# Kernel optimization log

Hardware: AMD Instinct MI355X
Metric: run time of the kernel (lower is better)

Reference implementation:

```python
import jax, jax.numpy as jnp
import numpy as np

N_NODES = 50000
N_EDGES = 1600000
IN_C = 256
HID_C = 128
OUT_C = 16
HEADS = 8
NEG_SLOPE = 0.2  # PyG GATConv default


def gat_layer(x, src, dst, W, att_src, att_dst, bias, heads, out_c):
    """PyG-style GATConv (eval mode, add_self_loops already applied to src/dst).
    x: [N, F_in], W: [F_in, heads*out_c], att_*: [heads, out_c], bias: [heads*out_c].
    Returns concatenated heads: [N, heads*out_c]."""
    N = x.shape[0]
    h = (x @ W).reshape(N, heads, out_c)                  # [N, H, C]
    a_src = (h * att_src[None]).sum(-1)                   # [N, H]
    a_dst = (h * att_dst[None]).sum(-1)                   # [N, H]
    alpha = a_src[src] + a_dst[dst]                       # [E, H]
    alpha = jax.nn.leaky_relu(alpha, NEG_SLOPE)
    # segment softmax over incoming edges of each destination node
    amax = jax.ops.segment_max(alpha, dst, num_segments=N)  # [N, H]
    alpha = jnp.exp(alpha - jax.lax.stop_gradient(amax)[dst])
    denom = jax.ops.segment_sum(alpha, dst, num_segments=N)  # [N, H]
    w = alpha / denom[dst]                                # [E, H]
    msg = h[src] * w[:, :, None]                          # [E, H, C]
    out = jax.ops.segment_sum(msg, dst, num_segments=N)   # [N, H, C]
    return out.reshape(N, heads * out_c) + bias


def setup_inputs() -> dict:
    key = jax.random.key(0)
    ks = jax.random.split(key, 10)
    x = jax.random.normal(ks[0], (N_NODES, IN_C), dtype=jnp.float32)
    edge_index = jax.random.randint(ks[1], (2, N_EDGES), 0, N_NODES, dtype=jnp.int32)
    c1 = HID_C // HEADS  # 16 per head
    s1 = 1.0 / np.sqrt(IN_C)
    s2 = 1.0 / np.sqrt(HID_C)
    return {
        "x": x,
        "edge_index": edge_index,
        "W1": jax.random.normal(ks[2], (IN_C, HEADS * c1), dtype=jnp.float32) * s1,
        "att_src1": jax.random.normal(ks[3], (HEADS, c1), dtype=jnp.float32) * s1,
        "att_dst1": jax.random.normal(ks[4], (HEADS, c1), dtype=jnp.float32) * s1,
        "bias1": jnp.zeros((HEADS * c1,), dtype=jnp.float32),
        "W2": jax.random.normal(ks[5], (HID_C, OUT_C), dtype=jnp.float32) * s2,
        "att_src2": jax.random.normal(ks[6], (1, OUT_C), dtype=jnp.float32) * s2,
        "att_dst2": jax.random.normal(ks[7], (1, OUT_C), dtype=jnp.float32) * s2,
        "bias2": jnp.zeros((OUT_C,), dtype=jnp.float32),
    }


def reference(x, edge_index, W1, att_src1, att_dst1, bias1, W2, att_src2, att_dst2, bias2):
    N = x.shape[0]
    loop = jnp.arange(N, dtype=edge_index.dtype)
    src = jnp.concatenate([edge_index[0], loop])  # add_self_loops=True (PyG default)
    dst = jnp.concatenate([edge_index[1], loop])
    h = gat_layer(x, src, dst, W1, att_src1, att_dst1, bias1, HEADS, HID_C // HEADS)
    h = jax.nn.relu(h)
    # F.dropout with training=False is identity (eval mode)
    out = gat_layer(h, src, dst, W2, att_src2, att_dst2, bias2, 1, OUT_C)
    return out
```

## Files before the change

kernel.cpp:

```cpp
#include <hip/hip_runtime.h>
#include <hip/hip_bf16.h>


#define NN 50000
#define NE 1600000
#define NBK 196
#define NB_SC 512
#define CHUNK (NE / NB_SC)
#define GB1 782
#define GB2 1563

typedef __attribute__((ext_vector_type(8))) short bf16x8;
typedef __attribute__((ext_vector_type(4))) float f32x4;

__device__ __forceinline__ float lrelu(float x) { return fmaxf(x, 0.2f * x); }

__device__ __forceinline__ float ldf(const void* p, int i, int isbf) {
  return isbf ? __bfloat162float(((const __hip_bfloat16*)p)[i])
              : ((const float*)p)[i];
}
__device__ __forceinline__ short f2bf_bits(float v) {
  __hip_bfloat16 h = __float2bfloat16(v);
  return *reinterpret_cast<short*>(&h);
}
__device__ __forceinline__ float bfs2f(short b) {
  unsigned int u = ((unsigned int)(unsigned short)b) << 16;
  union { unsigned int u; float f; } c; c.u = u; return c.f;
}
__device__ __forceinline__ unsigned short f2h_bits(float v) {
  _Float16 h = (_Float16)v;
  return *reinterpret_cast<unsigned short*>(&h);
}
__device__ __forceinline__ float h2f(unsigned short b) {
  _Float16 h = *reinterpret_cast<_Float16*>(&b);
  return (float)h;
}

#define OFF_H1   ((size_t)0)
#define OFF_H    ((size_t)25600000)
#define OFF_H2   ((size_t)51200000)
#define OFF_AS1  ((size_t)54400000)
#define OFF_AD1  ((size_t)56000000)
#define OFF_AS2  ((size_t)57600000)
#define OFF_AD2  ((size_t)57800000)
#define OFF_CNT  ((size_t)58000000)
#define OFF_OFFS ((size_t)58400000)
#define OFF_CSR  ((size_t)58600000)
#define OFF_WP1  ((size_t)65000000)
#define OFF_TOT  ((size_t)65065536)
#define OFF_FLAG ((size_t)65068608)

__global__ void repack_w1(const void* __restrict__ W1, short* __restrict__ Wp,
                          const unsigned int* __restrict__ xw, int* __restrict__ flag) {
  __shared__ int s[256];
  __shared__ int sf;
  int t = threadIdx.x;
  unsigned int w = xw[t * 97 + 5];
  unsigned int e = (w >> 7) & 0xFF;
  s[t] = (e >= 116 && e <= 138) ? 1 : 0;
  __syncthreads();
  for (int off = 128; off > 0; off >>= 1) {
    if (t < off) s[t] += s[t + off];
    __syncthreads();
  }
  if (t == 0) {
    sf = (s[0] >= 128) ? 1 : 0;
    if (blockIdx.x == 0) *flag = sf;
  }
  __syncthreads();
  int f = sf;
  int i = blockIdx.x * 256 + t;
  int j = i & 7, q = (i >> 3) & 3, c = (i >> 5) & 127, tt = i >> 12;
  int src = (tt * 32 + q * 8 + j) * 128 + c;
  Wp[i] = f ? ((const short*)W1)[src] : f2bf_bits(((const float*)W1)[src]);
}

__global__ __launch_bounds__(256) void fat1(const void* __restrict__ X,
                                            const short* __restrict__ Wp,
                                            short* __restrict__ H1b,
                                            const int* __restrict__ flag,
                                            const int* __restrict__ dst,
                                            int* __restrict__ HB) {
  __shared__ int h[224];
  if (blockIdx.x < GB1) {
    int wave = threadIdx.x >> 6, lane = threadIdx.x & 63;
    int rowbase = blockIdx.x * 64 + wave * 16;
    int l15 = lane & 15, quad = lane >> 4;
    int f = *flag;
    int arow = rowbase + l15;
    if (arow >= NN) arow = NN - 1;
    f32x4 acc[8];
#pragma unroll
    for (int ct = 0; ct < 8; ++ct) acc[ct] = (f32x4){0.f, 0.f, 0.f, 0.f};
    size_t abase = (size_t)arow * 256 + quad * 8;
#pragma unroll
    for (int kt = 0; kt < 8; ++kt) {
      bf16x8 a;
      if (f) {
        a = *(const bf16x8*)((const short*)X + abase + kt * 32);
      } else {
        const float* xp = (const float*)X + abase + kt * 32;
        float4 v0 = *(const float4*)xp, v1 = *(const float4*)(xp + 4);
        a[0] = f2bf_bits(v0.x); a[1] = f2bf_bits(v0.y);
        a[2] = f2bf_bits(v0.z); a[3] = f2bf_bits(v0.w);
        a[4] = f2bf_bits(v1.x); a[5] = f2bf_bits(v1.y);
        a[6] = f2bf_bits(v1.z); a[7] = f2bf_bits(v1.w);
      }
#pragma unroll
      for (int ct = 0; ct < 8; ++ct) {
        bf16x8 b = *(const bf16x8*)(Wp + ((kt * 128 + ct * 16 + l15) * 4 + quad) * 8);
        acc[ct] = __builtin_amdgcn_mfma_f32_16x16x32_bf16(a, b, acc[ct], 0, 0, 0);
      }
    }
    int r0 = rowbase + quad * 4;
#pragma unroll
    for (int ct = 0; ct < 8; ++ct)
#pragma unroll
      for (int r = 0; r < 4; ++r) {
        int row = r0 + r;
        if (row < NN) H1b[(size_t)row * 128 + ct * 16 + l15] = f2bf_bits(acc[ct][r]);
      }
  } else {
    int b = blockIdx.x - GB1;
    int t = threadIdx.x;
    for (int i = t; i < 224; i += 256) h[i] = 0;
    __syncthreads();
    int e0 = b * CHUNK, e1 = e0 + CHUNK;
    for (int e = e0 + t; e < e1; e += 256) atomicAdd(&h[dst[e] >> 8], 1);
    __syncthreads();
    for (int i = t; i < NBK; i += 256) HB[b * NBK + i] = h[i];
  }
}

__global__ __launch_bounds__(256) void fat2(const short* __restrict__ H1b,
                                            const void* __restrict__ as1,
                                            const void* __restrict__ ad1,
                                            float* __restrict__ AS,
                                            float* __restrict__ AD,
                                            const int* __restrict__ flag,
                                            int* __restrict__ HB,
                                            int* __restrict__ total) {
  __shared__ float s_as[128], s_ad[128];
  __shared__ int ts[256];
  int t = threadIdx.x;
  if (blockIdx.x < GB2) {
    int f = *flag;
    if (t < 128) { s_as[t] = ldf(as1, t, f); s_ad[t] = ldf(ad1, t, f); }
    __syncthreads();
    int tid = blockIdx.x * 256 + t;
    if (tid >= NN * 8) return;
    int n = tid >> 3, hh = tid & 7;
    const bf16x8* hp = (const bf16x8*)(H1b + (size_t)n * 128 + hh * 16);
    bf16x8 v0 = hp[0], v1 = hp[1];
    float as = 0.f, ad = 0.f;
#pragma unroll
    for (int i = 0; i < 8; ++i) {
      int b = hh * 16 + i;
      float x0 = bfs2f(v0[i]), x1 = bfs2f(v1[i]);
      as += x0 * s_as[b] + x1 * s_as[b + 8];
      ad += x0 * s_ad[b] + x1 * s_ad[b + 8];
    }
    AS[tid] = as; AD[tid] = ad;
  } else {
    int k = blockIdx.x - GB2;
    int v0 = HB[(t * 2) * NBK + k], v1 = HB[(t * 2 + 1) * NBK + k];
    int s = v0 + v1;
    ts[t] = s;
    __syncthreads();
    for (int off = 1; off < 256; off <<= 1) {
      int a = (t >= off) ? ts[t - off] : 0;
      __syncthreads();
      ts[t] += a;
      __syncthreads();
    }
    int ex = ts[t] - s;
    HB[(t * 2) * NBK + k] = ex;
    HB[(t * 2 + 1) * NBK + k] = ex + v0;
    if (t == 255) total[k] = ts[255];
  }
}

__global__ __launch_bounds__(256) void scat_write(const int* __restrict__ src,
                                                  const int* __restrict__ dst,
                                                  const int* __restrict__ HB,
                                                  const int* __restrict__ total,
                                                  unsigned int* __restrict__ EPp) {
  __shared__ int h[224], sc[256], lofs[224], lc[224], gd[224];
  __shared__ unsigned int EB[CHUNK];
  __shared__ unsigned char BKT[CHUNK];
  int t = threadIdx.x, b = blockIdx.x;
  int tv = (t < NBK) ? total[t] : 0;
  sc[t] = tv;
  __syncthreads();
  for (int off = 1; off < 256; off <<= 1) {
    int a = (t >= off) ? sc[t - off] : 0;
    __syncthreads();
    sc[t] += a;
    __syncthreads();
  }
  if (t < NBK) gd[t] = (sc[t] - tv) + HB[b * NBK + t];
  for (int i = t; i < 224; i += 256) h[i] = 0;
  __syncthreads();
  int e0 = b * CHUNK, e1 = e0 + CHUNK;
  for (int e = e0 + t; e < e1; e += 256) atomicAdd(&h[dst[e] >> 8], 1);
  __syncthreads();
  int v = (t < NBK) ? h[t] : 0;
  sc[t] = v;
  __syncthreads();
  for (int off = 1; off < 256; off <<= 1) {
    int a = (t >= off) ? sc[t - off] : 0;
    __syncthreads();
    sc[t] += a;
    __syncthreads();
  }
  if (t < NBK) { int ex = sc[t] - v; lofs[t] = ex; lc[t] = ex; }
  __syncthreads();
  for (int e = e0 + t; e < e1; e += 256) {
    int d = dst[e];
    int k = d >> 8;
    int pos = atomicAdd(&lc[k], 1);
    EB[pos] = ((unsigned int)(d & 255) << 16) | (unsigned int)src[e];
    BKT[pos] = (unsigned char)k;
  }
  __syncthreads();
  for (int pos = t; pos < CHUNK; pos += 256) {
    int k = BKT[pos];
    EPp[gd[k] + (pos - lofs[k])] = EB[pos];
  }
}

__global__ __launch_bounds__(1024) void bucket_csr(const unsigned int* __restrict__ EPp,
                                                   const int* __restrict__ total,
                                                   int* __restrict__ cnt,
                                                   int* __restrict__ offs,
                                                   unsigned short* __restrict__ csr) {
  __shared__ int h[256], sc[256], lc[256];
  int b = blockIdx.x, t = threadIdx.x;
  int tv = 0;
  if (t < 256) { tv = (t < NBK) ? total[t] : 0; sc[t] = tv; }
  __syncthreads();
  for (int off = 1; off < 256; off <<= 1) {
    int a = (t >= off && t < 256) ? sc[t - off] : 0;
    __syncthreads();
    if (t < 256) sc[t] += a;
    __syncthreads();
  }
  __shared__ int s_gbase, s_n;
  if (t == (unsigned)b) { s_gbase = sc[b] - tv; s_n = tv; }
  __syncthreads();
  int gbase = s_gbase, n = s_n;
  if (t < 256) h[t] = 0;
  __syncthreads();
  for (int i = t; i < n; i += 1024) atomicAdd(&h[(EPp[gbase + i] >> 16) & 255], 1);
  __syncthreads();
  int v = 0;
  if (t < 256) { v = h[t]; sc[t] = v; }
  __syncthreads();
  for (int off = 1; off < 256; off <<= 1) {
    int add = (t >= off && t < 256) ? sc[t - off] : 0;
    __syncthreads();
    if (t < 256) sc[t] += add;
    __syncthreads();
  }
  if (t < 256) {
    int ex = sc[t] - v;
    int node = (b << 8) + t;
    if (node < NN) { cnt[node] = v; offs[node] = gbase + ex; }
    lc[t] = ex;
  }
  __syncthreads();
  for (int i = t; i < n; i += 1024) {
    unsigned int p = EPp[gbase + i];
    int pos = atomicAdd(&lc[(p >> 16) & 255], 1);
    csr[gbase + pos] = (unsigned short)(p & 0xFFFF);
  }
}

__global__ __launch_bounds__(256) void agg1(const short* __restrict__ H1b,
                                            const float* __restrict__ AS,
                                            const float* __restrict__ AD,
                                            const int* __restrict__ offs,
                                            const int* __restrict__ cnt,
                                            const unsigned short* __restrict__ csr,
                                            const void* __restrict__ bias1,
                                            short* __restrict__ Hb,
                                            const int* __restrict__ flag) {
  int lane = threadIdx.x & 63;
  int node = blockIdx.x * 4 + (threadIdx.x >> 6);
  int f = *flag;
  int start = offs[node], deg = cnt[node];
  int g = lane >> 3, k = lane & 7;
  float adst = AD[node * 8 + k];
  float acc[16];
#pragma unroll
  for (int i = 0; i < 16; ++i) acc[i] = 0.f;
  float dsum = 0.f;
  if (g == 0) {
    float p = __expf(lrelu(AS[node * 8 + k] + adst));
    dsum = p;
    const bf16x8* hp = (const bf16x8*)(H1b + (size_t)node * 128 + k * 16);
    bf16x8 v0 = hp[0], v1 = hp[1];
#pragma unroll
    for (int i = 0; i < 8; ++i) {
      acc[i] = p * bfs2f(v0[i]);
      acc[8 + i] = p * bfs2f(v1[i]);
    }
  }
  int s = (g < deg) ? (int)csr[start + g] : -1;
  float a_c = 0.f; bf16x8 v0, v1;
  if (s >= 0) {
    a_c = AS[s * 8 + k];
    const bf16x8* hp = (const bf16x8*)(H1b + (size_t)s * 128 + k * 16);
    v0 = hp[0]; v1 = hp[1];
  }
  for (int eb = 0; eb < deg; eb += 8) {
    int en = eb + 8 + g;
    int sn = (en < deg) ? (int)csr[start + en] : -1;
    float a_n = 0.f; bf16x8 w0, w1;
    if (sn >= 0) {
      a_n = AS[sn * 8 + k];
      const bf16x8* hp = (const bf16x8*)(H1b + (size_t)sn * 128 + k * 16);
      w0 = hp[0]; w1 = hp[1];
    }
    if (s >= 0) {
      float p = __expf(lrelu(a_c + adst));
      dsum += p;
#pragma unroll
      for (int i = 0; i < 8; ++i) {
        acc[i] += p * bfs2f(v0[i]);
        acc[8 + i] += p * bfs2f(v1[i]);
      }
    }
    s = sn; a_c = a_n; v0 = w0; v1 = w1;
  }
#pragma unroll
  for (int i = 0; i < 16; ++i) {
    acc[i] += __shfl_xor(acc[i], 8);
    acc[i] += __shfl_xor(acc[i], 16);
    acc[i] += __shfl_xor(acc[i], 32);
  }
  dsum += __shfl_xor(dsum, 8);
  dsum += __shfl_xor(dsum, 16);
  dsum += __shfl_xor(dsum, 32);
  if (g == 0) {
    float inv = 1.0f / dsum;
    int c0 = k * 16;
    bf16x8 o0, o1;
#pragma unroll
    for (int i = 0; i < 8; ++i) {
      o0[i] = f2bf_bits(fmaxf(acc[i] * inv + ldf(bias1, c0 + i, f), 0.f));
      o1[i] = f2bf_bits(fmaxf(acc[8 + i] * inv + ldf(bias1, c0 + 8 + i, f), 0.f));
    }
    *(bf16x8*)(Hb + (size_t)node * 128 + c0) = o0;
    *(bf16x8*)(Hb + (size_t)node * 128 + c0 + 8) = o1;
  }
}

__global__ __launch_bounds__(256) void gemm2_a2(const short* __restrict__ Hb,
                                                const void* __restrict__ W2,
                                                const void* __restrict__ as2,
                                                const void* __restrict__ ad2,
                                                unsigned short* __restrict__ H2h,
                                                float* __restrict__ AS2,
                                                float* __restrict__ AD2,
                                                const int* __restrict__ flag) {
  __shared__ float sW[2048];
  __shared__ float s_as[16], s_ad[16];
  int t = threadIdx.x;
  int f = *flag;
  for (int i = t; i < 2048; i += 256) sW[i] = ldf(W2, i, f);
  if (t < 16) { s_as[t] = ldf(as2, t, f); s_ad[t] = ldf(ad2, t, f); }
  __syncthreads();
  int n = blockIdx.x * 16 + (t >> 4), c = t & 15;
  const bf16x8* hp = (const bf16x8*)(Hb + (size_t)n * 128);
  float acc = 0.f;
#pragma unroll 4
  for (int k8 = 0; k8 < 16; ++k8) {
    bf16x8 v = hp[k8];
#pragma unroll
    for (int i = 0; i < 8; ++i) acc += bfs2f(v[i]) * sW[(k8 * 8 + i) * 16 + c];
  }
  H2h[n * 16 + c] = f2h_bits(acc);
  float vs = acc * s_as[c], vd = acc * s_ad[c];
#pragma unroll
  for (int off = 1; off < 16; off <<= 1) {
    vs += __shfl_xor(vs, off);
    vd += __shfl_xor(vd, off);
  }
  if (c == 0) { AS2[n] = vs; AD2[n] = vd; }
}

__global__ __launch_bounds__(256) void agg2(const unsigned short* __restrict__ H2h,
                                            const float* __restrict__ AS2,
                                            const float* __restrict__ AD2,
                                            const int* __restrict__ offs,
                                            const int* __restrict__ cnt,
                                            const unsigned short* __restrict__ csr,
                                            const void* __restrict__ bias2,
                                            void* __restrict__ outv,
                                            const int* __restrict__ flag) {
  int lane = threadIdx.x & 63;
  int node = blockIdx.x * 4 + (threadIdx.x >> 6);
  int f = *flag;
  int start = offs[node], deg = cnt[node];
  int g = lane >> 3, k = lane & 7;
  float adst = AD2[node];
  float a0 = 0.f, a1 = 0.f, dsum = 0.f;
  if (g == 0) {
    float p = __expf(lrelu(AS2[node] + adst));
    dsum = p;
    unsigned int hv = *(const unsigned int*)(H2h + (size_t)node * 16 + k * 2);
    a0 = p * h2f((unsigned short)(hv & 0xFFFF));
    a1 = p * h2f((unsigned short)(hv >> 16));
  }
  int s = (g < deg) ? (int)csr[start + g] : -1;
  float as_c = 0.f; unsigned int hv_c = 0;
  if (s >= 0) {
    as_c = AS2[s];
    hv_c = *(const unsigned int*)(H2h + (size_t)s * 16 + k * 2);
  }
  for (int eb = 0; eb < deg; eb += 8) {
    int en = eb + 8 + g;
    int sn = (en < deg) ? (int)csr[start + en] : -1;
    float as_n = 0.f; unsigned int hv_n = 0;
    if (sn >= 0) {
      as_n = AS2[sn];
      hv_n = *(const unsigned int*)(H2h + (size_t)sn * 16 + k * 2);
    }
    if (s >= 0) {
      float p = __expf(lrelu(as_c + adst));
      dsum += p;
      a0 += p * h2f((unsigned short)(hv_c & 0xFFFF));
      a1 += p * h2f((unsigned short)(hv_c >> 16));
    }
    s = sn; as_c = as_n; hv_c = hv_n;
  }
  a0 += __shfl_xor(a0, 8);  a0 += __shfl_xor(a0, 16);  a0 += __shfl_xor(a0, 32);
  a1 += __shfl_xor(a1, 8);  a1 += __shfl_xor(a1, 16);  a1 += __shfl_xor(a1, 32);
  dsum += __shfl_xor(dsum, 8); dsum += __shfl_xor(dsum, 16); dsum += __shfl_xor(dsum, 32);
  if (g == 0) {
    float inv = 1.0f / dsum;
    float o0 = a0 * inv + ldf(bias2, k * 2 + 0, f);
    float o1 = a1 * inv + ldf(bias2, k * 2 + 1, f);
    size_t base = (size_t)node * 16 + k * 2;
    if (f) {
      ((__hip_bfloat16*)outv)[base] = __float2bfloat16(o0);
      ((__hip_bfloat16*)outv)[base + 1] = __float2bfloat16(o1);
    } else {
      *(float2*)((float*)outv + base) = make_float2(o0, o1);
    }
  }
}

extern "C" void kernel_launch(void* const* d_in, const int* in_sizes, int n_in,
                              void* d_out, int out_size, void* d_ws, size_t ws_size,
                              hipStream_t stream) {
  const void* x = d_in[0];
  const int* ei = (const int*)d_in[1];
  const void* W1 = d_in[2];
  const void* as1 = d_in[3];
  const void* ad1 = d_in[4];
  const void* b1 = d_in[5];
  const void* W2 = d_in[6];
  const void* as2 = d_in[7];
  const void* ad2 = d_in[8];
  const void* b2 = d_in[9];
  char* ws = (char*)d_ws;

  short* H1b = (short*)(ws + OFF_H1);
  short* Hb = (short*)(ws + OFF_H);
  unsigned int* EPp = (unsigned int*)(ws + OFF_H);
  unsigned short* H2h = (unsigned short*)(ws + OFF_H2);
  int* HB = (int*)(ws + OFF_H2);
  float* AS1 = (float*)(ws + OFF_AS1);
  float* AD1 = (float*)(ws + OFF_AD1);
  float* AS2 = (float*)(ws + OFF_AS2);
  float* AD2 = (float*)(ws + OFF_AD2);
  int* CNT = (int*)(ws + OFF_CNT);
  int* OFFS = (int*)(ws + OFF_OFFS);
  unsigned short* CSR = (unsigned short*)(ws + OFF_CSR);
  short* Wp = (short*)(ws + OFF_WP1);
  int* TOT = (int*)(ws + OFF_TOT);
  int* FLAG = (int*)(ws + OFF_FLAG);

  repack_w1<<<128, 256, 0, stream>>>(W1, Wp, (const unsigned int*)x, FLAG);
  fat1<<<GB1 + NB_SC, 256, 0, stream>>>(x, Wp, H1b, FLAG, ei + NE, HB);
  fat2<<<GB2 + NBK, 256, 0, stream>>>(H1b, as1, ad1, AS1, AD1, FLAG, HB, TOT);
  scat_write<<<NB_SC, 256, 0, stream>>>(ei, ei + NE, HB, TOT, EPp);
  bucket_csr<<<NBK, 1024, 0, stream>>>(EPp, TOT, CNT, OFFS, CSR);

  agg1<<<NN / 4, 256, 0, stream>>>(H1b, AS1, AD1, OFFS, CNT, CSR, b1, Hb, FLAG);
  gemm2_a2<<<NN / 16, 256, 0, stream>>>(Hb, W2, as2, ad2, H2h, AS2, AD2, FLAG);
  agg2<<<NN / 4, 256, 0, stream>>>(H2h, AS2, AD2, OFFS, CNT, CSR, b2, d_out, FLAG);
}
```

Baseline: 273.4 us.

## Fuse layer-2 linear transform and attention logits into layer-1 aggregation epilogue

Merges the gemm2_a2 kernel into the layer-1 aggregation kernel, so each node's ReLU'd hidden vector is multiplied by W2 in registers and reduced with wave shuffles. This removes the bf16 hidden-feature buffer write and reread plus one kernel launch. Each block now stages W2, bias1 and the attention vectors into shared memory, which adds per-block setup traffic and register pressure. The hidden features also stay in fp32 rather than being rounded to bf16 before the second GEMM.

```diff
diff --git a/kernel.cpp b/kernel.cpp
--- a/kernel.cpp
+++ b/kernel.cpp
@@ -276,18 +276,30 @@
   }
 }
 
-__global__ __launch_bounds__(256) void agg1(const short* __restrict__ H1b,
-                                            const float* __restrict__ AS,
-                                            const float* __restrict__ AD,
-                                            const int* __restrict__ offs,
-                                            const int* __restrict__ cnt,
-                                            const unsigned short* __restrict__ csr,
-                                            const void* __restrict__ bias1,
-                                            short* __restrict__ Hb,
-                                            const int* __restrict__ flag) {
-  int lane = threadIdx.x & 63;
-  int node = blockIdx.x * 4 + (threadIdx.x >> 6);
+__global__ __launch_bounds__(256) void agg1f(const short* __restrict__ H1b,
+                                             const float* __restrict__ AS,
+                                             const float* __restrict__ AD,
+                                             const int* __restrict__ offs,
+                                             const int* __restrict__ cnt,
+                                             const unsigned short* __restrict__ csr,
+                                             const void* __restrict__ bias1,
+                                             const void* __restrict__ W2,
+                                             const void* __restrict__ as2,
+                                             const void* __restrict__ ad2,
+                                             unsigned short* __restrict__ H2h,
+                                             float* __restrict__ AS2,
+                                             float* __restrict__ AD2,
+                                             const int* __restrict__ flag) {
+  __shared__ float sW[2048];
+  __shared__ float sB[128], s_as[16], s_ad[16];
+  int t = threadIdx.x;
   int f = *flag;
+  for (int i = t; i < 2048; i += 256) sW[i] = ldf(W2, i, f);
+  if (t < 128) sB[t] = ldf(bias1, t, f);
+  if (t < 16) { s_as[t] = ldf(as2, t, f); s_ad[t] = ldf(ad2, t, f); }
+  __syncthreads();
+  int lane = t & 63;
+  int node = blockIdx.x * 4 + (t >> 6);
   int start = offs[node], deg = cnt[node];
   int g = lane >> 3, k = lane & 7;
   float adst = AD[node * 8 + k];
@@ -299,11 +311,11 @@
     float p = __expf(lrelu(AS[node * 8 + k] + adst));
     dsum = p;
     const bf16x8* hp = (const bf16x8*)(H1b + (size_t)node * 128 + k * 16);
-    bf16x8 v0 = hp[0], v1 = hp[1];
+    bf16x8 v0s = hp[0], v1s = hp[1];
 #pragma unroll
     for (int i = 0; i < 8; ++i) {
-      acc[i] = p * bfs2f(v0[i]);
-      acc[8 + i] = p * bfs2f(v1[i]);
+      acc[i] = p * bfs2f(v0s[i]);
+      acc[8 + i] = p * bfs2f(v1s[i]);
     }
   }
   int s = (g < deg) ? (int)csr[start + g] : -1;
@@ -342,52 +354,30 @@
   dsum += __shfl_xor(dsum, 8);
   dsum += __shfl_xor(dsum, 16);
   dsum += __shfl_xor(dsum, 32);
-  if (g == 0) {
-    float inv = 1.0f / dsum;
-    int c0 = k * 16;
-    bf16x8 o0, o1;
-#pragma unroll
-    for (int i = 0; i < 8; ++i) {
-      o0[i] = f2bf_bits(fmaxf(acc[i] * inv + ldf(bias1, c0 + i, f), 0.f));
-      o1[i] = f2bf_bits(fmaxf(acc[8 + i] * inv + ldf(bias1, c0 + 8 + i, f), 0.f));
-    }
-    *(bf16x8*)(Hb + (size_t)node * 128 + c0) = o0;
-    *(bf16x8*)(Hb + (size_t)node * 128 + c0 + 8) = o1;
-  }
-}
-
-__global__ __launch_bounds__(256) void gemm2_a2(const short* __restrict__ Hb,
-                                                const void* __restrict__ W2,
-                                                const void* __restrict__ as2,
-                                                const void* __restrict__ ad2,
-                                                unsigned short* __restrict__ H2h,
-                                                float* __restrict__ AS2,
-                                                float* __restrict__ AD2,
-                                                const int* __restrict__ flag) {
-  __shared__ float sW[2048];
-  __shared__ float s_as[16], s_ad[16];
-  int t = threadIdx.x;
-  int f = *flag;
-  for (int i = t; i < 2048; i += 256) sW[i] = ldf(W2, i, f);
-  if (t < 16) { s_as[t] = ldf(as2, t, f); s_ad[t] = ldf(ad2, t, f); }
-  __syncthreads();
-  int n = blockIdx.x * 16 + (t >> 4), c = t & 15;
-  const bf16x8* hp = (const bf16x8*)(Hb + (size_t)n * 128);
-  float acc = 0.f;
-#pragma unroll 4
-  for (int k8 = 0; k8 < 16; ++k8) {
-    bf16x8 v = hp[k8];
-#pragma unroll
-    for (int i = 0; i < 8; ++i) acc += bfs2f(v[i]) * sW[(k8 * 8 + i) * 16 + c];
-  }
-  H2h[n * 16 + c] = f2h_bits(acc);
-  float vs = acc * s_as[c], vd = acc * s_ad[c];
-#pragma unroll
-  for (int off = 1; off < 16; off <<= 1) {
-    vs += __shfl_xor(vs, off);
-    vd += __shfl_xor(vd, off);
-  }
-  if (c == 0) { AS2[n] = vs; AD2[n] = vd; }
+  float inv = 1.0f / dsum;
+  int c0 = k * 16;
+  float h[16];
+#pragma unroll
+  for (int i = 0; i < 16; ++i) h[i] = fmaxf(acc[i] * inv + sB[c0 + i], 0.f);
+  int cc = g * 2;
+  float p0 = 0.f, p1 = 0.f;
+#pragma unroll
+  for (int i = 0; i < 16; ++i) {
+    float w0v = sW[(c0 + i) * 16 + cc], w1v = sW[(c0 + i) * 16 + cc + 1];
+    p0 += h[i] * w0v;
+    p1 += h[i] * w1v;
+  }
+  p0 += __shfl_xor(p0, 1); p0 += __shfl_xor(p0, 2); p0 += __shfl_xor(p0, 4);
+  p1 += __shfl_xor(p1, 1); p1 += __shfl_xor(p1, 2); p1 += __shfl_xor(p1, 4);
+  if (k == 0) {
+    unsigned int packed = (unsigned int)f2h_bits(p0) | ((unsigned int)f2h_bits(p1) << 16);
+    ((unsigned int*)H2h)[node * 8 + g] = packed;
+  }
+  float vs = p0 * s_as[cc] + p1 * s_as[cc + 1];
+  float vd = p0 * s_ad[cc] + p1 * s_ad[cc + 1];
+  vs += __shfl_xor(vs, 8); vs += __shfl_xor(vs, 16); vs += __shfl_xor(vs, 32);
+  vd += __shfl_xor(vd, 8); vd += __shfl_xor(vd, 16); vd += __shfl_xor(vd, 32);
+  if (lane == 0) { AS2[node] = vs; AD2[node] = vd; }
 }
 
 __global__ __launch_bounds__(256) void agg2(const unsigned short* __restrict__ H2h,
@@ -468,7 +458,6 @@
   char* ws = (char*)d_ws;
 
   short* H1b = (short*)(ws + OFF_H1);
-  short* Hb = (short*)(ws + OFF_H);
   unsigned int* EPp = (unsigned int*)(ws + OFF_H);
   unsigned short* H2h = (unsigned short*)(ws + OFF_H2);
   int* HB = (int*)(ws + OFF_H2);
@@ -489,7 +478,7 @@
   scat_write<<<NB_SC, 256, 0, stream>>>(ei, ei + NE, HB, TOT, EPp);
   bucket_csr<<<NBK, 1024, 0, stream>>>(EPp, TOT, CNT, OFFS, CSR);
 
-  agg1<<<NN / 4, 256, 0, stream>>>(H1b, AS1, AD1, OFFS, CNT, CSR, b1, Hb, FLAG);
-  gemm2_a2<<<NN / 16, 256, 0, stream>>>(Hb, W2, as2, ad2, H2h, AS2, AD2, FLAG);
+  agg1f<<<NN / 4, 256, 0, stream>>>(H1b, AS1, AD1, OFFS, CNT, CSR, b1,
+                                    W2, as2, ad2, H2h, AS2, AD2, FLAG);
   agg2<<<NN / 4, 256, 0, stream>>>(H2h, AS2, AD2, OFFS, CNT, CSR, b2, d_out, FLAG);
 }
```

After: 296.8 us. 1.09x slower.
